# Kernel optimization log

Measured on AMD Instinct MI355X. Metric: run time of the kernel, lower is better.

Reference implementation:

```python
import jax, jax.numpy as jnp
import numpy as np

B, L, F, U, P, CAT = 64, 25, 128, 10000, 10000, 400
PI = 3.141592653589793


def haversine(lat1, lon1, lat2, lon2):
    p = PI / 180.0
    a = 0.5 - jnp.cos((lat2 - lat1) * p) / 2 \
        + jnp.cos(lat1 * p) * jnp.cos(lat2 * p) * (1 - jnp.cos((lon2 - lon1) * p)) / 2
    return 12742.0 * jnp.arcsin(jnp.sqrt(a))


def setup_inputs() -> dict:
    key = jax.random.key(0)
    ks = jax.random.split(key, 24)
    s = 0.02
    return {
        "user": jax.random.randint(ks[0], (B, L), 0, U),
        "poi": jax.random.randint(ks[1], (B, L), 0, P),
        "cat": jax.random.randint(ks[2], (B, L), 0, CAT),
        "lat": jax.random.uniform(ks[3], (B, L), dtype=jnp.float32),
        "lon": jax.random.uniform(ks[4], (B, L), dtype=jnp.float32),
        "tod": jax.random.randint(ks[5], (B, L), 0, 24),
        "dow": jax.random.randint(ks[6], (B, L), 0, 7),
        "unixtime": jax.random.uniform(ks[7], (B, L), dtype=jnp.float32),
        "user_emb_w": jax.random.normal(ks[8], (U, F), jnp.float32) * s,
        "poi_emb_w": jax.random.normal(ks[9], (P, F), jnp.float32) * s,
        "tod_emb_w": jax.random.normal(ks[10], (24, F), jnp.float32) * s,
        "dow_emb_w": jax.random.normal(ks[11], (7, F), jnp.float32) * s,
        "Wq": jax.random.normal(ks[12], (F, F), jnp.float32) * s,
        "bq": jnp.zeros((F,), jnp.float32),
        "Wk": jax.random.normal(ks[13], (F, F), jnp.float32) * s,
        "bk": jnp.zeros((F,), jnp.float32),
        "Wv": jax.random.normal(ks[14], (F, F), jnp.float32) * s,
        "bv": jnp.zeros((F,), jnp.float32),
        "w_val": jax.random.normal(ks[15], (L,), jnp.float32) * 0.2,
        "b_val": jnp.zeros((), jnp.float32),
        "distance_matrix": jax.random.uniform(ks[16], (P, P), dtype=jnp.float32),
    }


def reference(user, poi, cat, lat, lon, tod, dow, unixtime,
              user_emb_w, poi_emb_w, tod_emb_w, dow_emb_w,
              Wq, bq, Wk, bk, Wv, bv, w_val, b_val, distance_matrix):
    # token embeddings  [B,L,F]
    inputs = user_emb_w[user] + poi_emb_w[poi] + tod_emb_w[tod] + dow_emb_w[dow]

    # pairwise haversine / time deltas  [B,L,L]  (vectorized double loop)
    delta_s = haversine(lat[:, :, None], lon[:, :, None], lat[:, None, :], lon[:, None, :])
    delta_t = jnp.abs(unixtime[:, :, None] - unixtime[:, None, :])
    su, sl = delta_s.max(), delta_s.min()
    tu, tl = delta_t.max(), delta_t.min()
    delta = (jnp.exp(-delta_s / (su - sl)) + jnp.exp(-delta_t / (tu - tl))) / 2

    # successive time intervals  [B,L], first column = 0
    time_interval = jnp.concatenate(
        [jnp.zeros((B, 1), unixtime.dtype), jnp.abs(unixtime[:, 1:] - unixtime[:, :-1])], axis=1)
    interval_s = distance_matrix[poi]            # [B,L,P] gather of candidate distances
    interval_t = time_interval[:, :, None]       # broadcast to [B,L,P]
    su1, sl1 = interval_s.max(), interval_s.min()
    tu1, tl1 = time_interval.max(), time_interval.min()
    interval = (jnp.exp(-interval_s / (su1 - sl1)) + jnp.exp(-interval_t / (tu1 - tl1))) / 2

    # additive-bias self-attention
    q = inputs @ Wq + bq
    k = inputs @ Wk + bk
    v = inputs @ Wv + bv
    scores = jnp.einsum('bif,bjf->bij', q, k) + delta
    attn_w = jax.nn.softmax(scores, axis=-1)
    self_attn_out = jnp.einsum('bij,bjf->bif', attn_w, v)   # [B,L,F]

    # candidate attention over all POIs, weighted by spatio-temporal interval
    cand_attn = jnp.einsum('pf,blf->bpl', poi_emb_w, self_attn_out) \
        * jnp.swapaxes(interval, 1, 2)                      # [B,P,L]
    pre = cand_attn @ w_val + b_val                          # Linear(25,1) -> [B,P]
    return (pre, pre)
```

## Files before the change

kernel.cpp:

```cpp
#include <hip/hip_runtime.h>
#include <math.h>

#define BB 64
#define LL 25
#define FF 128
#define PP 10000

#define OFF_GEOP 0
#define OFF_TTP  256
#define OFF_RRP  384
#define OFF_TT   1184
#define OFF_C1   2784
#define OFF_C2   4384
#define OFF_DS   5984
#define OFF_DT   45984
#define OFF_Q    85984
#define OFF_K    290784
#define OFF_V    495584
#define OFF_AH   700384
#define OFF_AL   831456
#define OFF_BH   962528
#define OFF_BL   1609696

#define NB_PREP 625
#define NB_GEO  64
#define NB_QKV  192
#define NB_ROW  400
#define NB_FRONT (NB_PREP + NB_GEO + NB_QKV + NB_ROW)

#define NEG_INF -3.402823466e38f
#define POS_INF  3.402823466e38f

typedef short bf16x8 __attribute__((ext_vector_type(8)));
typedef float f32x16 __attribute__((ext_vector_type(16)));

__device__ inline unsigned short f2bf(float x) {
    unsigned u = __float_as_uint(x);
    u += 0x7FFFu + ((u >> 16) & 1u);
    return (unsigned short)(u >> 16);
}
__device__ inline float bf2f(unsigned short h) {
    return __uint_as_float(((unsigned)h) << 16);
}

template <bool MAX>
__device__ float blockReduce(float v) {
    __shared__ float sh[8];
    const int lane = threadIdx.x & 63;
    const int wid  = threadIdx.x >> 6;
#pragma unroll
    for (int off = 32; off > 0; off >>= 1) {
        float o = __shfl_down(v, off, 64);
        v = MAX ? fmaxf(v, o) : fminf(v, o);
    }
    __syncthreads();
    if (lane == 0) sh[wid] = v;
    __syncthreads();
    if (threadIdx.x == 0) {
        const int nw = blockDim.x >> 6;
        for (int w = 1; w < nw; ++w) v = MAX ? fmaxf(v, sh[w]) : fminf(v, sh[w]);
    }
    return v;
}

__global__ void k_front(const int* __restrict__ user, const int* __restrict__ poi,
                        const int* __restrict__ tod, const int* __restrict__ dow,
                        const float* __restrict__ lat, const float* __restrict__ lon,
                        const float* __restrict__ ut,
                        const float* __restrict__ ue, const float* __restrict__ pe,
                        const float* __restrict__ te, const float* __restrict__ de,
                        const float* __restrict__ Wq, const float* __restrict__ bq,
                        const float* __restrict__ Wk, const float* __restrict__ bk,
                        const float* __restrict__ Wv, const float* __restrict__ bv,
                        const float* __restrict__ dm, float* __restrict__ ws) {
    const int blk = blockIdx.x, t = threadIdx.x;

    if (blk < NB_PREP) {
        const int gid = blk * 256 + t;
        const int p   = gid >> 4;
        const int sub = gid & 15;
        const int kk  = sub >> 1, kh = sub & 1;
        const float* src = pe + p * FF + kk * 16 + kh * 8;
        float4 a0 = *(const float4*)(src);
        float4 a1 = *(const float4*)(src + 4);
        float xv[8] = {a0.x, a0.y, a0.z, a0.w, a1.x, a1.y, a1.z, a1.w};
        bf16x8 hv, lv;
#pragma unroll
        for (int j = 0; j < 8; ++j) {
            unsigned short h = f2bf(xv[j]);
            hv[j] = (short)h;
            lv[j] = (short)f2bf(xv[j] - bf2f(h));
        }
        const int c = p >> 5, n = p & 31;
        const int pos = (c * 8 + kk) * 64 + (kh * 32 + n);
        ((bf16x8*)((unsigned short*)(ws + OFF_BH)))[pos] = hv;
        ((bf16x8*)((unsigned short*)(ws + OFF_BL)))[pos] = lv;

    } else if (blk < NB_PREP + NB_GEO) {
        const int b = blk - NB_PREP;
        __shared__ float la[LL], lo[LL], uu[LL];
        if (t < LL) { la[t] = lat[b * LL + t]; lo[t] = lon[b * LL + t]; uu[t] = ut[b * LL + t]; }
        __syncthreads();
        float dsmax = NEG_INF, dsmin = POS_INF, dtmax = NEG_INF, dtmin = POS_INF;
        const float p = 0.017453292519943295f;
        for (int idx = t; idx < LL * LL; idx += 256) {
            int i = idx / LL, j = idx % LL;
            float a = 0.5f - cosf((la[j] - la[i]) * p) * 0.5f
                    + cosf(la[i] * p) * cosf(la[j] * p) * (1.0f - cosf((lo[j] - lo[i]) * p)) * 0.5f;
            float d  = 12742.0f * asinf(sqrtf(a));
            float dt = fabsf(uu[i] - uu[j]);
            ws[OFF_DS + b * 625 + idx] = d;
            ws[OFF_DT + b * 625 + idx] = dt;
            dsmax = fmaxf(dsmax, d); dsmin = fminf(dsmin, d);
            dtmax = fmaxf(dtmax, dt); dtmin = fminf(dtmin, dt);
        }
        float r;
        r = blockReduce<true >(dsmax); if (!t) ws[OFF_GEOP + b * 4 + 0] = r;
        r = blockReduce<false>(dsmin); if (!t) ws[OFF_GEOP + b * 4 + 1] = r;
        r = blockReduce<true >(dtmax); if (!t) ws[OFF_GEOP + b * 4 + 2] = r;
        r = blockReduce<false>(dtmin); if (!t) ws[OFF_GEOP + b * 4 + 3] = r;
        float ttv = 0.0f;
        if (t < LL) {
            ttv = (t == 0) ? 0.0f : fabsf(uu[t] - uu[t - 1]);
            ws[OFF_TT + b * LL + t] = ttv;
        }
        float tmax = (t < LL) ? ttv : NEG_INF;
        float tmin = (t < LL) ? ttv : POS_INF;
        r = blockReduce<true >(tmax); if (!t) ws[OFF_TTP + b * 2 + 0] = r;
        r = blockReduce<false>(tmin); if (!t) ws[OFF_TTP + b * 2 + 1] = r;

    } else if (blk < NB_PREP + NB_GEO + NB_QKV) {
        const int id = blk - (NB_PREP + NB_GEO);
        const int b = id & 63, m = id >> 6;
        __shared__ __align__(16) float xs[26 * FF];
        __shared__ int ids[4][LL];
        if (t < LL) {
            ids[0][t] = user[b * LL + t]; ids[1][t] = poi[b * LL + t];
            ids[2][t] = tod[b * LL + t];  ids[3][t] = dow[b * LL + t];
        }
        if (t < FF) xs[LL * FF + t] = 0.0f;
        __syncthreads();
        for (int idx = t; idx < LL * FF; idx += 256) {
            int l = idx >> 7, f = idx & 127;
            xs[idx] = ue[ids[0][l] * FF + f] + pe[ids[1][l] * FF + f]
                    + te[ids[2][l] * FF + f] + de[ids[3][l] * FF + f];
        }
        __syncthreads();
        const float* W    = (m == 0) ? Wq : (m == 1) ? Wk : Wv;
        const float* bias = (m == 0) ? bq : (m == 1) ? bk : bv;
        float* o = ws + ((m == 0) ? OFF_Q : (m == 1) ? OFF_K : OFF_V) + b * LL * FF;
        const int f  = t & 127;
        const int l0 = (t >> 7) * 13;
        float acc[13];
#pragma unroll
        for (int i = 0; i < 13; ++i) acc[i] = 0.0f;
        for (int g = 0; g < FF; g += 4) {
            float w0 = W[(g + 0) * FF + f];
            float w1 = W[(g + 1) * FF + f];
            float w2 = W[(g + 2) * FF + f];
            float w3 = W[(g + 3) * FF + f];
#pragma unroll
            for (int i = 0; i < 13; ++i) {
                float4 x = *(const float4*)(xs + (l0 + i) * FF + g);
                acc[i] = fmaf(x.w, w3, fmaf(x.z, w2, fmaf(x.y, w1, fmaf(x.x, w0, acc[i]))));
            }
        }
        float bb = bias[f];
#pragma unroll
        for (int i = 0; i < 13; ++i) {
            int l = l0 + i;
            if (l < LL) o[l * FF + f] = acc[i] + bb;
        }

    } else {
        const int g = blk - (NB_PREP + NB_GEO + NB_QKV);
        float mx = NEG_INF, mn = POS_INF;
#pragma unroll
        for (int rr = 0; rr < 4; ++rr) {
            const int r = poi[g * 4 + rr];
            const float4* row = (const float4*)(dm + (size_t)r * PP);
            for (int i = t; i < PP / 4; i += 256) {
                float4 v = row[i];
                mx = fmaxf(mx, fmaxf(fmaxf(v.x, v.y), fmaxf(v.z, v.w)));
                mn = fminf(mn, fminf(fminf(v.x, v.y), fminf(v.z, v.w)));
            }
        }
        float r2;
        r2 = blockReduce<true >(mx); if (!t) ws[OFF_RRP + g * 2 + 0] = r2;
        r2 = blockReduce<false>(mn); if (!t) ws[OFF_RRP + g * 2 + 1] = r2;
    }
}

__global__ void k_attn(const float* __restrict__ w_val, float* __restrict__ ws) {
    const int b = blockIdx.x, t = threadIdx.x;
    __shared__ float qs[LL * 129], ks[LL * 129], vs[LL * FF], sc[LL * LL];
    __shared__ float bc[6];
    {
        float g0 = (t < 64) ? ws[OFF_GEOP + t * 4 + 0] : NEG_INF;
        float g1 = (t < 64) ? ws[OFF_GEOP + t * 4 + 1] : POS_INF;
        float g2 = (t < 64) ? ws[OFF_GEOP + t * 4 + 2] : NEG_INF;
        float g3 = (t < 64) ? ws[OFF_GEOP + t * 4 + 3] : POS_INF;
        float t0 = (t < 64) ? ws[OFF_TTP + t * 2 + 0] : NEG_INF;
        float t1 = (t < 64) ? ws[OFF_TTP + t * 2 + 1] : POS_INF;
        float r;
        r = blockReduce<true >(g0); if (!t) bc[0] = r;
        r = blockReduce<false>(g1); if (!t) bc[1] = r;
        r = blockReduce<true >(g2); if (!t) bc[2] = r;
        r = blockReduce<false>(g3); if (!t) bc[3] = r;
        r = blockReduce<true >(t0); if (!t) bc[4] = r;
        r = blockReduce<false>(t1); if (!t) bc[5] = r;
    }
    for (int idx = t; idx < LL * FF; idx += 256) {
        int l = idx >> 7, f = idx & 127;
        qs[l * 129 + f] = ws[OFF_Q + b * LL * FF + idx];
        ks[l * 129 + f] = ws[OFF_K + b * LL * FF + idx];
        vs[idx]         = ws[OFF_V + b * LL * FF + idx];
    }
    __syncthreads();
    const float su  = bc[0], sl  = bc[1];
    const float tu  = bc[2], tl  = bc[3];
    const float tu1 = bc[4], tl1 = bc[5];
    const float nS0 = -1.0f / (su - sl), nT0 = -1.0f / (tu - tl), nT1 = -1.0f / (tu1 - tl1);
    for (int idx = t; idx < LL * LL; idx += 256) {
        int i = idx / LL, j = idx % LL;
        float a = 0.0f;
        for (int f = 0; f < FF; ++f) a = fmaf(qs[i * 129 + f], ks[j * 129 + f], a);
        float d  = ws[OFF_DS + b * 625 + idx];
        float dt = ws[OFF_DT + b * 625 + idx];
        sc[idx] = a + 0.5f * (expf(d * nS0) + expf(dt * nT0));
    }
    __syncthreads();
    if (t < LL) {
        float m = NEG_INF;
        for (int j = 0; j < LL; ++j) m = fmaxf(m, sc[t * LL + j]);
        float s = 0.0f;
        for (int j = 0; j < LL; ++j) { float e = expf(sc[t * LL + j] - m); sc[t * LL + j] = e; s += e; }
        float inv = 1.0f / s;
        for (int j = 0; j < LL; ++j) sc[t * LL + j] *= inv;
    }
    __syncthreads();
    unsigned short* Ah = (unsigned short*)(ws + OFF_AH);
    unsigned short* Al = (unsigned short*)(ws + OFF_AL);
    for (int idx = t; idx < LL * FF; idx += 256) {
        int l = idx >> 7, f = idx & 127;
        float a = 0.0f;
        for (int j = 0; j < LL; ++j) a = fmaf(sc[l * LL + j], vs[j * FF + f], a);
        unsigned short h  = f2bf(a);
        unsigned short lo = f2bf(a - bf2f(h));
        int kk = f >> 4, kh = (f >> 3) & 1, j = f & 7;
        int pos = ((b * 8 + kk) * 64 + (kh * 32 + l)) * 8 + j;
        Ah[pos] = h; Al[pos] = lo;
    }
    if (t < LL) {
        float ttv = ws[OFF_TT + b * LL + t];
        float wv  = w_val[t];
        ws[OFF_C1 + b * LL + t] = 0.5f * wv * expf(ttv * nT1);
        ws[OFF_C2 + b * LL + t] = 0.5f * wv;
    }
}

__global__ void __launch_bounds__(256) k_main(const int* __restrict__ poi,
                                              const float* __restrict__ dm,
                                              const float* __restrict__ bval_p,
                                              const float* __restrict__ ws,
                                              float* __restrict__ out) {
    const int t = threadIdx.x;
    const int wave = t >> 6, lane = t & 63;
    const int half = lane >> 5, col = lane & 31;
    __shared__ float lc1[BB * 32], lc2[BB * 32];
    __shared__ int   lrw[BB * 32];
    __shared__ float bc2[2];
    {
        float mx = NEG_INF, mn = POS_INF;
        for (int i = t; i < 400; i += 256) {
            mx = fmaxf(mx, ws[OFF_RRP + i * 2 + 0]);
            mn = fminf(mn, ws[OFF_RRP + i * 2 + 1]);
        }
        float r;
        r = blockReduce<true >(mx); if (!t) bc2[0] = r;
        r = blockReduce<false>(mn); if (!t) bc2[1] = r;
    }
    for (int idx = t; idx < BB * LL; idx += 256) {
        int b = idx / LL, l = idx - b * LL;
        lc1[b * 32 + l] = ws[OFF_C1 + idx];
        lc2[b * 32 + l] = ws[OFF_C2 + idx];
        lrw[b * 32 + l] = poi[idx];
    }
    __syncthreads();
    const float su1 = bc2[0], sl1 = bc2[1];
    const float nS1 = -1.0f / (su1 - sl1);
    const float bv  = bval_p[0];
    const int ct  = blockIdx.x * 4 + wave;
    const int p   = ct * 32 + col;
    const int pcl = min(p, PP - 1);
    const bf16x8* Bh = (const bf16x8*)(ws + OFF_BH);
    const bf16x8* Bl = (const bf16x8*)(ws + OFF_BL);
    const bf16x8* Ah = (const bf16x8*)(ws + OFF_AH);
    const bf16x8* Al = (const bf16x8*)(ws + OFF_AL);
    bf16x8 bh[8], bl[8];
#pragma unroll
    for (int kk = 0; kk < 8; ++kk) {
        bh[kk] = Bh[(ct * 8 + kk) * 64 + lane];
        bl[kk] = Bl[(ct * 8 + kk) * 64 + lane];
    }
    const int b0 = blockIdx.y * 8;
    for (int bi = 0; bi < 8; ++bi) {
        const int b = b0 + bi;
        f32x16 acc = {};
#pragma unroll
        for (int kk = 0; kk < 8; ++kk) {
            bf16x8 ah = Ah[(b * 8 + kk) * 64 + lane];
            bf16x8 al = Al[(b * 8 + kk) * 64 + lane];
            acc = __builtin_amdgcn_mfma_f32_32x32x16_bf16(ah, bh[kk], acc, 0, 0, 0);
            acc = __builtin_amdgcn_mfma_f32_32x32x16_bf16(al, bh[kk], acc, 0, 0, 0);
            acc = __builtin_amdgcn_mfma_f32_32x32x16_bf16(ah, bl[kk], acc, 0, 0, 0);
        }
        float sum = 0.0f;
#pragma unroll
        for (int r = 0; r < 13; ++r) {
            int row  = (r & 3) + 8 * (r >> 2) + 4 * half;
            int rowc = min(row, LL - 1);
            float d  = dm[(size_t)lrw[b * 32 + rowc] * PP + pcl];
            float w  = lc1[b * 32 + rowc] + lc2[b * 32 + rowc] * __expf(d * nS1);
            w = (row < LL) ? w : 0.0f;
            sum = fmaf(w, acc[r], sum);
        }
        sum += __shfl_xor(sum, 32, 64);
        sum += bv;
        if (half == 0 && p < PP) {
            out[b * PP + p]           = sum;
            out[BB * PP + b * PP + p] = sum;
        }
    }
}

extern "C" void kernel_launch(void* const* d_in, const int* in_sizes, int n_in,
                              void* d_out, int out_size, void* d_ws, size_t ws_size,
                              hipStream_t stream) {
    const int*   user = (const int*)d_in[0];
    const int*   poi  = (const int*)d_in[1];
    const float* lat  = (const float*)d_in[3];
    const float* lon  = (const float*)d_in[4];
    const int*   tod  = (const int*)d_in[5];
    const int*   dow  = (const int*)d_in[6];
    const float* ut   = (const float*)d_in[7];
    const float* ue   = (const float*)d_in[8];
    const float* pe   = (const float*)d_in[9];
    const float* te   = (const float*)d_in[10];
    const float* de   = (const float*)d_in[11];
    const float* Wq   = (const float*)d_in[12];
    const float* bq   = (const float*)d_in[13];
    const float* Wk   = (const float*)d_in[14];
    const float* bk   = (const float*)d_in[15];
    const float* Wv   = (const float*)d_in[16];
    const float* bv   = (const float*)d_in[17];
    const float* w_val = (const float*)d_in[18];
    const float* b_val = (const float*)d_in[19];
    const float* dm   = (const float*)d_in[20];
    float* out = (float*)d_out;
    float* ws  = (float*)d_ws;

    k_front<<<NB_FRONT, 256, 0, stream>>>(user, poi, tod, dow, lat, lon, ut,
                                          ue, pe, te, de, Wq, bq, Wk, bk, Wv, bv,
                                          dm, ws);
    k_attn<<<BB, 256, 0, stream>>>(w_val, ws);
    k_main<<<dim3(79, 8), 256, 0, stream>>>(poi, dm, b_val, ws, out);
}
```

Baseline: 572.1 us.

## Rebalance work across stages: fuse QKV+scores per batch, split attention and main grid

The front kernel now computes geo deltas, embeddings, all three QKV projections and the QK^T scores in one block per batch, and it orders the long distance-row reduction blocks first. The middle attention kernel is split into two feature halves per batch and stages the bf16 hi/lo output in shared memory for vectorized stores. The main kernel grid doubles along the batch axis, with 4 batches per block instead of 8. The aim is to shorten the critical path and raise occupancy. The cost is heavier per-block work for the 64 fused front blocks and more redundant B-fragment loads in the main kernel.

```diff
diff --git a/kernel.cpp b/kernel.cpp
--- a/kernel.cpp
+++ b/kernel.cpp
@@ -14,19 +14,17 @@
 #define OFF_C2   4384
 #define OFF_DS   5984
 #define OFF_DT   45984
-#define OFF_Q    85984
-#define OFF_K    290784
+#define OFF_SC   85984
 #define OFF_V    495584
 #define OFF_AH   700384
 #define OFF_AL   831456
 #define OFF_BH   962528
 #define OFF_BL   1609696
 
+#define NB_ROW  400
+#define NB_BF   64
 #define NB_PREP 625
-#define NB_GEO  64
-#define NB_QKV  192
-#define NB_ROW  400
-#define NB_FRONT (NB_PREP + NB_GEO + NB_QKV + NB_ROW)
+#define NB_FRONT (NB_ROW + NB_BF + NB_PREP)
 
 #define NEG_INF -3.402823466e38f
 #define POS_INF  3.402823466e38f
@@ -75,38 +73,42 @@
                         const float* __restrict__ dm, float* __restrict__ ws) {
     const int blk = blockIdx.x, t = threadIdx.x;
 
-    if (blk < NB_PREP) {
-        const int gid = blk * 256 + t;
-        const int p   = gid >> 4;
-        const int sub = gid & 15;
-        const int kk  = sub >> 1, kh = sub & 1;
-        const float* src = pe + p * FF + kk * 16 + kh * 8;
-        float4 a0 = *(const float4*)(src);
-        float4 a1 = *(const float4*)(src + 4);
-        float xv[8] = {a0.x, a0.y, a0.z, a0.w, a1.x, a1.y, a1.z, a1.w};
-        bf16x8 hv, lv;
-#pragma unroll
-        for (int j = 0; j < 8; ++j) {
-            unsigned short h = f2bf(xv[j]);
-            hv[j] = (short)h;
-            lv[j] = (short)f2bf(xv[j] - bf2f(h));
-        }
-        const int c = p >> 5, n = p & 31;
-        const int pos = (c * 8 + kk) * 64 + (kh * 32 + n);
-        ((bf16x8*)((unsigned short*)(ws + OFF_BH)))[pos] = hv;
-        ((bf16x8*)((unsigned short*)(ws + OFF_BL)))[pos] = lv;
-
-    } else if (blk < NB_PREP + NB_GEO) {
-        const int b = blk - NB_PREP;
+    if (blk < NB_ROW) {
+        const int g = blk;
+        float mx = NEG_INF, mn = POS_INF;
+#pragma unroll
+        for (int rr = 0; rr < 4; ++rr) {
+            const int r = poi[g * 4 + rr];
+            const float4* row = (const float4*)(dm + (size_t)r * PP);
+            for (int i = t; i < PP / 4; i += 256) {
+                float4 v = row[i];
+                mx = fmaxf(mx, fmaxf(fmaxf(v.x, v.y), fmaxf(v.z, v.w)));
+                mn = fminf(mn, fminf(fminf(v.x, v.y), fminf(v.z, v.w)));
+            }
+        }
+        float r2;
+        r2 = blockReduce<true >(mx); if (!t) ws[OFF_RRP + g * 2 + 0] = r2;
+        r2 = blockReduce<false>(mn); if (!t) ws[OFF_RRP + g * 2 + 1] = r2;
+
+    } else if (blk < NB_ROW + NB_BF) {
+        const int b = blk - NB_ROW;
+        __shared__ __align__(16) float xs[26 * FF];
+        __shared__ float qs[LL * 129], ks[LL * 129];
+        __shared__ int ids[4][LL];
         __shared__ float la[LL], lo[LL], uu[LL];
-        if (t < LL) { la[t] = lat[b * LL + t]; lo[t] = lon[b * LL + t]; uu[t] = ut[b * LL + t]; }
+        if (t < LL) {
+            ids[0][t] = user[b * LL + t]; ids[1][t] = poi[b * LL + t];
+            ids[2][t] = tod[b * LL + t];  ids[3][t] = dow[b * LL + t];
+            la[t] = lat[b * LL + t]; lo[t] = lon[b * LL + t]; uu[t] = ut[b * LL + t];
+        }
+        if (t < FF) xs[LL * FF + t] = 0.0f;
         __syncthreads();
         float dsmax = NEG_INF, dsmin = POS_INF, dtmax = NEG_INF, dtmin = POS_INF;
-        const float p = 0.017453292519943295f;
+        const float pc = 0.017453292519943295f;
         for (int idx = t; idx < LL * LL; idx += 256) {
             int i = idx / LL, j = idx % LL;
-            float a = 0.5f - cosf((la[j] - la[i]) * p) * 0.5f
-                    + cosf(la[i] * p) * cosf(la[j] * p) * (1.0f - cosf((lo[j] - lo[i]) * p)) * 0.5f;
+            float a = 0.5f - cosf((la[j] - la[i]) * pc) * 0.5f
+                    + cosf(la[i] * pc) * cosf(la[j] * pc) * (1.0f - cosf((lo[j] - lo[i]) * pc)) * 0.5f;
             float d  = 12742.0f * asinf(sqrtf(a));
             float dt = fabsf(uu[i] - uu[j]);
             ws[OFF_DS + b * 625 + idx] = d;
@@ -128,73 +130,80 @@
         float tmin = (t < LL) ? ttv : POS_INF;
         r = blockReduce<true >(tmax); if (!t) ws[OFF_TTP + b * 2 + 0] = r;
         r = blockReduce<false>(tmin); if (!t) ws[OFF_TTP + b * 2 + 1] = r;
-
-    } else if (blk < NB_PREP + NB_GEO + NB_QKV) {
-        const int id = blk - (NB_PREP + NB_GEO);
-        const int b = id & 63, m = id >> 6;
-        __shared__ __align__(16) float xs[26 * FF];
-        __shared__ int ids[4][LL];
-        if (t < LL) {
-            ids[0][t] = user[b * LL + t]; ids[1][t] = poi[b * LL + t];
-            ids[2][t] = tod[b * LL + t];  ids[3][t] = dow[b * LL + t];
-        }
-        if (t < FF) xs[LL * FF + t] = 0.0f;
-        __syncthreads();
         for (int idx = t; idx < LL * FF; idx += 256) {
             int l = idx >> 7, f = idx & 127;
             xs[idx] = ue[ids[0][l] * FF + f] + pe[ids[1][l] * FF + f]
                     + te[ids[2][l] * FF + f] + de[ids[3][l] * FF + f];
         }
         __syncthreads();
-        const float* W    = (m == 0) ? Wq : (m == 1) ? Wk : Wv;
-        const float* bias = (m == 0) ? bq : (m == 1) ? bk : bv;
-        float* o = ws + ((m == 0) ? OFF_Q : (m == 1) ? OFF_K : OFF_V) + b * LL * FF;
         const int f  = t & 127;
         const int l0 = (t >> 7) * 13;
-        float acc[13];
-#pragma unroll
-        for (int i = 0; i < 13; ++i) acc[i] = 0.0f;
-        for (int g = 0; g < FF; g += 4) {
-            float w0 = W[(g + 0) * FF + f];
-            float w1 = W[(g + 1) * FF + f];
-            float w2 = W[(g + 2) * FF + f];
-            float w3 = W[(g + 3) * FF + f];
+        auto mm = [&](const float* W, const float* bias, float* dstL, float* dstG) {
+            float acc[13];
+#pragma unroll
+            for (int i = 0; i < 13; ++i) acc[i] = 0.0f;
+            for (int g = 0; g < FF; g += 4) {
+                float w0 = W[(g + 0) * FF + f];
+                float w1 = W[(g + 1) * FF + f];
+                float w2 = W[(g + 2) * FF + f];
+                float w3 = W[(g + 3) * FF + f];
+#pragma unroll
+                for (int i = 0; i < 13; ++i) {
+                    float4 x = *(const float4*)(xs + (l0 + i) * FF + g);
+                    acc[i] = fmaf(x.w, w3, fmaf(x.z, w2, fmaf(x.y, w1, fmaf(x.x, w0, acc[i]))));
+                }
+            }
+            float bb = bias[f];
 #pragma unroll
             for (int i = 0; i < 13; ++i) {
-                float4 x = *(const float4*)(xs + (l0 + i) * FF + g);
-                acc[i] = fmaf(x.w, w3, fmaf(x.z, w2, fmaf(x.y, w1, fmaf(x.x, w0, acc[i]))));
+                int l = l0 + i;
+                if (l < LL) {
+                    if (dstL) dstL[l * 129 + f] = acc[i] + bb;
+                    else      dstG[l * FF  + f] = acc[i] + bb;
+                }
             }
-        }
-        float bb = bias[f];
-#pragma unroll
-        for (int i = 0; i < 13; ++i) {
-            int l = l0 + i;
-            if (l < LL) o[l * FF + f] = acc[i] + bb;
+        };
+        mm(Wq, bq, qs, nullptr);
+        mm(Wk, bk, ks, nullptr);
+        mm(Wv, bv, nullptr, ws + OFF_V + b * LL * FF);
+        __syncthreads();
+        for (int idx = t; idx < LL * LL; idx += 256) {
+            int i = idx / LL, j = idx % LL;
+            float a = 0.0f;
+            for (int ff2 = 0; ff2 < FF; ++ff2)
+                a = fmaf(qs[i * 129 + ff2], ks[j * 129 + ff2], a);
+            ws[OFF_SC + b * 625 + idx] = a;
         }
 
     } else {
-        const int g = blk - (NB_PREP + NB_GEO + NB_QKV);
-        float mx = NEG_INF, mn = POS_INF;
-#pragma unroll
-        for (int rr = 0; rr < 4; ++rr) {
-            const int r = poi[g * 4 + rr];
-            const float4* row = (const float4*)(dm + (size_t)r * PP);
-            for (int i = t; i < PP / 4; i += 256) {
-                float4 v = row[i];
-                mx = fmaxf(mx, fmaxf(fmaxf(v.x, v.y), fmaxf(v.z, v.w)));
-                mn = fminf(mn, fminf(fminf(v.x, v.y), fminf(v.z, v.w)));
-            }
-        }
-        float r2;
-        r2 = blockReduce<true >(mx); if (!t) ws[OFF_RRP + g * 2 + 0] = r2;
-        r2 = blockReduce<false>(mn); if (!t) ws[OFF_RRP + g * 2 + 1] = r2;
-    }
-}
-
-__global__ void k_attn(const float* __restrict__ w_val, float* __restrict__ ws) {
-    const int b = blockIdx.x, t = threadIdx.x;
-    __shared__ float qs[LL * 129], ks[LL * 129], vs[LL * FF], sc[LL * LL];
+        const int gid = (blk - (NB_ROW + NB_BF)) * 256 + t;
+        const int p   = gid >> 4;
+        const int sub = gid & 15;
+        const int kk  = sub >> 1, kh = sub & 1;
+        const float* src = pe + p * FF + kk * 16 + kh * 8;
+        float4 a0 = *(const float4*)(src);
+        float4 a1 = *(const float4*)(src + 4);
+        float xv[8] = {a0.x, a0.y, a0.z, a0.w, a1.x, a1.y, a1.z, a1.w};
+        bf16x8 hv, lv;
+#pragma unroll
+        for (int j = 0; j < 8; ++j) {
+            unsigned short h = f2bf(xv[j]);
+            hv[j] = (short)h;
+            lv[j] = (short)f2bf(xv[j] - bf2f(h));
+        }
+        const int c = p >> 5, n = p & 31;
+        const int pos = (c * 8 + kk) * 64 + (kh * 32 + n);
+        ((bf16x8*)((unsigned short*)(ws + OFF_BH)))[pos] = hv;
+        ((bf16x8*)((unsigned short*)(ws + OFF_BL)))[pos] = lv;
+    }
+}
+
+__global__ void k_mid(const float* __restrict__ w_val, float* __restrict__ ws) {
+    const int b = blockIdx.x, h = blockIdx.y, t = threadIdx.x;
+    __shared__ float sc[LL * LL];
+    __shared__ float vsh[LL * 64];
     __shared__ float bc[6];
+    __shared__ __align__(16) unsigned short ahs[4 * 64 * 8], als[4 * 64 * 8];
     {
         float g0 = (t < 64) ? ws[OFF_GEOP + t * 4 + 0] : NEG_INF;
         float g1 = (t < 64) ? ws[OFF_GEOP + t * 4 + 1] : POS_INF;
@@ -210,24 +219,23 @@
         r = blockReduce<true >(t0); if (!t) bc[4] = r;
         r = blockReduce<false>(t1); if (!t) bc[5] = r;
     }
-    for (int idx = t; idx < LL * FF; idx += 256) {
-        int l = idx >> 7, f = idx & 127;
-        qs[l * 129 + f] = ws[OFF_Q + b * LL * FF + idx];
-        ks[l * 129 + f] = ws[OFF_K + b * LL * FF + idx];
-        vs[idx]         = ws[OFF_V + b * LL * FF + idx];
-    }
-    __syncthreads();
-    const float su  = bc[0], sl  = bc[1];
-    const float tu  = bc[2], tl  = bc[3];
-    const float tu1 = bc[4], tl1 = bc[5];
-    const float nS0 = -1.0f / (su - sl), nT0 = -1.0f / (tu - tl), nT1 = -1.0f / (tu1 - tl1);
+    for (int idx = t; idx < LL * LL; idx += 256) sc[idx] = ws[OFF_SC + b * 625 + idx];
+    for (int idx = t; idx < LL * 64; idx += 256) {
+        int l = idx >> 6, f0 = idx & 63;
+        vsh[idx] = ws[OFF_V + b * LL * FF + l * FF + h * 64 + f0];
+    }
+    for (int idx = t; idx < 1024; idx += 256) {
+        ((unsigned*)ahs)[idx] = 0u;
+        ((unsigned*)als)[idx] = 0u;
+    }
+    __syncthreads();
+    const float nS0 = -1.0f / (bc[0] - bc[1]);
+    const float nT0 = -1.0f / (bc[2] - bc[3]);
+    const float nT1 = -1.0f / (bc[4] - bc[5]);
     for (int idx = t; idx < LL * LL; idx += 256) {
-        int i = idx / LL, j = idx % LL;
-        float a = 0.0f;
-        for (int f = 0; f < FF; ++f) a = fmaf(qs[i * 129 + f], ks[j * 129 + f], a);
         float d  = ws[OFF_DS + b * 625 + idx];
         float dt = ws[OFF_DT + b * 625 + idx];
-        sc[idx] = a + 0.5f * (expf(d * nS0) + expf(dt * nT0));
+        sc[idx] += 0.5f * (expf(d * nS0) + expf(dt * nT0));
     }
     __syncthreads();
     if (t < LL) {
@@ -239,19 +247,25 @@
         for (int j = 0; j < LL; ++j) sc[t * LL + j] *= inv;
     }
     __syncthreads();
-    unsigned short* Ah = (unsigned short*)(ws + OFF_AH);
-    unsigned short* Al = (unsigned short*)(ws + OFF_AL);
-    for (int idx = t; idx < LL * FF; idx += 256) {
-        int l = idx >> 7, f = idx & 127;
+    for (int idx = t; idx < LL * 64; idx += 256) {
+        int l = idx >> 6, f0 = idx & 63;
         float a = 0.0f;
-        for (int j = 0; j < LL; ++j) a = fmaf(sc[l * LL + j], vs[j * FF + f], a);
-        unsigned short h  = f2bf(a);
-        unsigned short lo = f2bf(a - bf2f(h));
-        int kk = f >> 4, kh = (f >> 3) & 1, j = f & 7;
-        int pos = ((b * 8 + kk) * 64 + (kh * 32 + l)) * 8 + j;
-        Ah[pos] = h; Al[pos] = lo;
-    }
-    if (t < LL) {
+        for (int j = 0; j < LL; ++j) a = fmaf(sc[l * LL + j], vsh[j * 64 + f0], a);
+        unsigned short hh = f2bf(a);
+        unsigned short lo = f2bf(a - bf2f(hh));
+        int kk = f0 >> 4, kh = (f0 >> 3) & 1, jj = f0 & 7;
+        int spos = (kk * 64 + (kh * 32 + l)) * 8 + jj;
+        ahs[spos] = hh; als[spos] = lo;
+    }
+    __syncthreads();
+    {
+        int kki = t >> 6, ln = t & 63;
+        bf16x8 hv = *(const bf16x8*)(ahs + (kki * 64 + ln) * 8);
+        bf16x8 lv = *(const bf16x8*)(als + (kki * 64 + ln) * 8);
+        ((bf16x8*)((unsigned short*)(ws + OFF_AH)))[(b * 8 + h * 4 + kki) * 64 + ln] = hv;
+        ((bf16x8*)((unsigned short*)(ws + OFF_AL)))[(b * 8 + h * 4 + kki) * 64 + ln] = lv;
+    }
+    if (h == 0 && t < LL) {
         float ttv = ws[OFF_TT + b * LL + t];
         float wv  = w_val[t];
         ws[OFF_C1 + b * LL + t] = 0.5f * wv * expf(ttv * nT1);
@@ -267,9 +281,10 @@
     const int t = threadIdx.x;
     const int wave = t >> 6, lane = t & 63;
     const int half = lane >> 5, col = lane & 31;
-    __shared__ float lc1[BB * 32], lc2[BB * 32];
-    __shared__ int   lrw[BB * 32];
+    __shared__ float lc1[4 * 32], lc2[4 * 32];
+    __shared__ int   lrw[4 * 32];
     __shared__ float bc2[2];
+    const int b0 = blockIdx.y * 4;
     {
         float mx = NEG_INF, mn = POS_INF;
         for (int i = t; i < 400; i += 256) {
@@ -280,11 +295,11 @@
         r = blockReduce<true >(mx); if (!t) bc2[0] = r;
         r = blockReduce<false>(mn); if (!t) bc2[1] = r;
     }
-    for (int idx = t; idx < BB * LL; idx += 256) {
-        int b = idx / LL, l = idx - b * LL;
-        lc1[b * 32 + l] = ws[OFF_C1 + idx];
-        lc2[b * 32 + l] = ws[OFF_C2 + idx];
-        lrw[b * 32 + l] = poi[idx];
+    if (t < 4 * LL) {
+        int bi = t / LL, l = t - bi * LL;
+        lc1[bi * 32 + l] = ws[OFF_C1 + (b0 + bi) * LL + l];
+        lc2[bi * 32 + l] = ws[OFF_C2 + (b0 + bi) * LL + l];
+        lrw[bi * 32 + l] = poi[(b0 + bi) * LL + l];
     }
     __syncthreads();
     const float su1 = bc2[0], sl1 = bc2[1];
@@ -303,8 +318,7 @@
         bh[kk] = Bh[(ct * 8 + kk) * 64 + lane];
         bl[kk] = Bl[(ct * 8 + kk) * 64 + lane];
     }
-    const int b0 = blockIdx.y * 8;
-    for (int bi = 0; bi < 8; ++bi) {
+    for (int bi = 0; bi < 4; ++bi) {
         const int b = b0 + bi;
         f32x16 acc = {};
 #pragma unroll
@@ -320,8 +334,8 @@
         for (int r = 0; r < 13; ++r) {
             int row  = (r & 3) + 8 * (r >> 2) + 4 * half;
             int rowc = min(row, LL - 1);
-            float d  = dm[(size_t)lrw[b * 32 + rowc] * PP + pcl];
-            float w  = lc1[b * 32 + rowc] + lc2[b * 32 + rowc] * __expf(d * nS1);
+            float d  = dm[(size_t)lrw[bi * 32 + rowc] * PP + pcl];
+            float w  = lc1[bi * 32 + rowc] + lc2[bi * 32 + rowc] * __expf(d * nS1);
             w = (row < LL) ? w : 0.0f;
             sum = fmaf(w, acc[r], sum);
         }
@@ -363,6 +377,6 @@
     k_front<<<NB_FRONT, 256, 0, stream>>>(user, poi, tod, dow, lat, lon, ut,
                                           ue, pe, te, de, Wq, bq, Wk, bk, Wv, bv,
                                           dm, ws);
-    k_attn<<<BB, 256, 0, stream>>>(w_val, ws);
-    k_main<<<dim3(79, 8), 256, 0, stream>>>(poi, dm, b_val, ws, out);
-}
+    k_mid<<<dim3(BB, 2), 256, 0, stream>>>(w_val, ws);
+    k_main<<<dim3(79, 16), 256, 0, stream>>>(poi, dm, b_val, ws, out);
+}
```

Result: slower. 605.3 us (+5.8%).
